# Kernel tuning notes

Hardware: AMD Instinct MI355X
Metric: run time of the kernel (lower is better)

## Reference

```python
import jax, jax.numpy as jnp
import numpy as np

DIM = 256
HEADS = 8
WSZ = (2, 7, 7)
SSZ = (1, 3, 3)
EPS = 1e-5


def _rel_index(wsz):
    wt, wh, ww = wsz
    coords = np.stack(np.meshgrid(np.arange(wt), np.arange(wh), np.arange(ww), indexing='ij'))
    coords = coords.reshape(3, -1)  # (3, N)
    rel = coords[:, :, None] - coords[:, None, :]  # (3, N, N)
    rel = rel.transpose(1, 2, 0).copy()  # (N, N, 3)
    rel[:, :, 0] += wt - 1
    rel[:, :, 1] += wh - 1
    rel[:, :, 2] += ww - 1
    rel[:, :, 0] *= (2 * wh - 1) * (2 * ww - 1)
    rel[:, :, 1] *= (2 * ww - 1)
    return rel.sum(-1)  # (N, N) int


def _attn_mask_np(T, H, W, wsz, ssz):
    wt, wh, ww = wsz
    st, sh, sw = ssz
    img = np.zeros((T, H, W), np.int32)
    cnt = 0
    for t in (slice(0, -wt), slice(-wt, -st), slice(-st, None)):
        for h in (slice(0, -wh), slice(-wh, -sh), slice(-sh, None)):
            for w in (slice(0, -ww), slice(-ww, -sw), slice(-sw, None)):
                img[t, h, w] = cnt
                cnt += 1
    m = img.reshape(T // wt, wt, H // wh, wh, W // ww, ww)
    m = m.transpose(0, 2, 4, 1, 3, 5).reshape(-1, wt * wh * ww)  # (nW, N)
    diff = m[:, :, None] - m[:, None, :]
    return np.where(diff != 0, -100.0, 0.0).astype(np.float32)  # (nW, N, N)


def _ln(x, w, b):
    mu = x.mean(-1, keepdims=True)
    var = jnp.mean((x - mu) ** 2, -1, keepdims=True)
    return (x - mu) * jax.lax.rsqrt(var + EPS) * w + b


def _window_partition(x, wsz):
    B, T, H, W, C = x.shape
    wt, wh, ww = wsz
    x = x.reshape(B, T // wt, wt, H // wh, wh, W // ww, ww, C)
    x = x.transpose(0, 1, 3, 5, 2, 4, 6, 7)
    return x.reshape(-1, wt * wh * ww, C)


def _window_reverse(xw, wsz, B, T, H, W):
    wt, wh, ww = wsz
    C = xw.shape[-1]
    x = xw.reshape(B, T // wt, H // wh, W // ww, wt, wh, ww, C)
    x = x.transpose(0, 1, 4, 2, 5, 3, 6, 7)
    return x.reshape(B, T, H, W, C)


def setup_inputs() -> dict:
    key = jax.random.key(0)
    ks = jax.random.split(key, 8)
    B, T, H, W = 2, 8, 56, 56
    d = DIM
    hid = 4 * d
    rpe_rows = (2 * WSZ[0] - 1) * (2 * WSZ[1] - 1) * (2 * WSZ[2] - 1)
    s = 0.02
    return {
        'x': jax.random.normal(ks[0], (B, T, H, W, d), jnp.float32),
        'norm1_w': jnp.ones((d,), jnp.float32),
        'norm1_b': jnp.zeros((d,), jnp.float32),
        'qkv_w': jax.random.normal(ks[1], (3 * d, d), jnp.float32) * s,
        'qkv_b': jnp.zeros((3 * d,), jnp.float32),
        'proj_w': jax.random.normal(ks[2], (d, d), jnp.float32) * s,
        'proj_b': jnp.zeros((d,), jnp.float32),
        'rpe_table': jax.random.normal(ks[3], (rpe_rows, HEADS), jnp.float32) * s,
        'norm2_w': jnp.ones((d,), jnp.float32),
        'norm2_b': jnp.zeros((d,), jnp.float32),
        'fc1_w': jax.random.normal(ks[4], (hid, d), jnp.float32) * s,
        'fc1_b': jnp.zeros((hid,), jnp.float32),
        'fc2_w': jax.random.normal(ks[5], (d, hid), jnp.float32) * s,
        'fc2_b': jnp.zeros((d,), jnp.float32),
    }


def reference(x, norm1_w, norm1_b, qkv_w, qkv_b, proj_w, proj_b, rpe_table,
              norm2_w, norm2_b, fc1_w, fc1_b, fc2_w, fc2_b):
    B, T, H, W, C = x.shape
    wt, wh, ww = WSZ
    N = wt * wh * ww
    hd = C // HEADS
    scale = hd ** -0.5

    shortcut = x
    h = _ln(x, norm1_w, norm1_b)
    # shifted branch: cyclic roll + mask
    h = jnp.roll(h, (-SSZ[0], -SSZ[1], -SSZ[2]), axis=(1, 2, 3))
    mask = jnp.asarray(_attn_mask_np(T, H, W, WSZ, SSZ))  # (nW, N, N)
    nW = mask.shape[0]

    xw = _window_partition(h, WSZ)  # (B*nW, N, C)
    Bw = xw.shape[0]

    qkv = xw @ qkv_w.T + qkv_b  # (Bw, N, 3C)
    qkv = qkv.reshape(Bw, N, 3, HEADS, hd).transpose(2, 0, 3, 1, 4)
    q, k, v = qkv[0], qkv[1], qkv[2]  # (Bw, H, N, hd)

    idx = _rel_index(WSZ)  # (N, N)
    bias = rpe_table[idx].transpose(2, 0, 1)  # (heads, N, N)

    attn = jnp.einsum('bhnd,bhmd->bhnm', q * scale, k) + bias[None]
    attn = attn.reshape(B, nW, HEADS, N, N) + mask[None, :, None]
    attn = jax.nn.softmax(attn, axis=-1).reshape(Bw, HEADS, N, N)

    out = jnp.einsum('bhnm,bhmd->bhnd', attn, v)
    out = out.transpose(0, 2, 1, 3).reshape(Bw, N, C)
    out = out @ proj_w.T + proj_b

    out = _window_reverse(out, WSZ, B, T, H, W)
    out = jnp.roll(out, (SSZ[0], SSZ[1], SSZ[2]), axis=(1, 2, 3))

    x = shortcut + out
    h2 = _ln(x, norm2_w, norm2_b)
    h2 = jax.nn.gelu(h2 @ fc1_w.T + fc1_b, approximate=False)
    h2 = h2 @ fc2_w.T + fc2_b
    return x + h2
```

## Files before the change

kernel.cpp:

```cpp
#include <hip/hip_runtime.h>
#include <math.h>

#define TOKENS 50176
#define NWIN   512
#define C_DIM  256

typedef __attribute__((ext_vector_type(8))) short short8;
typedef __attribute__((ext_vector_type(4))) float f32x4;

__device__ __forceinline__ unsigned short f2bf(float f) {
    unsigned int u = __builtin_bit_cast(unsigned int, f);
    u += 0x7fffu + ((u >> 16) & 1);
    return (unsigned short)(u >> 16);
}

__device__ __forceinline__ void gll16(const void* g, void* l) {
    __builtin_amdgcn_global_load_lds(
        (const __attribute__((address_space(1))) unsigned int*)g,
        (__attribute__((address_space(3))) unsigned int*)l, 16, 0, 0);
}

__device__ __forceinline__ int win_token_to_flat(int u) {
    int g = u / 98;
    int n = u - g * 98;
    int bb  = g >> 8;
    int rem = g & 255;
    int tb = rem >> 6, hb = (rem >> 3) & 7, wb = rem & 7;
    int dt = n / 49;
    int r2 = n - dt * 49;
    int dh = r2 / 7, dw = r2 - dh * 7;
    int t = tb * 2 + dt, h = hb * 7 + dh, w = wb * 7 + dw;
    int ts = (t + 1) & 7;
    int hs = h + 3; if (hs >= 56) hs -= 56;
    int wsx = w + 3; if (wsx >= 56) wsx -= 56;
    return ((bb * 8 + ts) * 56 + hs) * 56 + wsx;
}

__global__ __launch_bounds__(256) void cvt_kernel(
        const float* __restrict__ src, unsigned short* __restrict__ dst, int n) {
    int i = blockIdx.x * 256 + threadIdx.x;
    if (i < n) dst[i] = f2bf(src[i]);
}

__global__ __launch_bounds__(256) void bm_kernel(
        const float* __restrict__ rpe, float* __restrict__ bm) {
    int i = blockIdx.x * 256 + threadIdx.x;
    int c  = i % 112;
    int t1 = i / 112;
    int r  = t1 % 112;
    int t2 = t1 / 112;
    int head = t2 & 7;
    int cls  = t2 >> 3;
    float val;
    if (c >= 98) {
        val = -1e30f;
    } else if (r >= 98) {
        val = 0.f;
    } else {
        int dt = r / 49, rr = r - dt * 49, dh = rr / 7, dw = rr - dh * 7;
        int dt2 = c / 49, cc = c - dt2 * 49, dh2 = cc / 7, dw2 = cc - dh2 * 7;
        int rt  = (cls & 4) ? (dt  == 0 ? 1 : 2) : 0;
        int rh  = (cls & 2) ? (dh  <  4 ? 1 : 2) : 0;
        int rw  = (cls & 1) ? (dw  <  4 ? 1 : 2) : 0;
        int rt2 = (cls & 4) ? (dt2 == 0 ? 1 : 2) : 0;
        int rh2 = (cls & 2) ? (dh2 <  4 ? 1 : 2) : 0;
        int rw2 = (cls & 1) ? (dw2 <  4 ? 1 : 2) : 0;
        int reg1 = rt * 9 + rh * 3 + rw, reg2 = rt2 * 9 + rh2 * 3 + rw2;
        int idx = (dt - dt2 + 1) * 169 + (dh - dh2 + 6) * 13 + (dw - dw2 + 6);
        val = rpe[idx * 8 + head] + ((reg1 == reg2) ? 0.f : -100.f);
    }
    bm[i] = val;
}

template<bool GATHER>
__global__ __launch_bounds__(256) void ln_kernel(
        const float* __restrict__ x, const float* __restrict__ w,
        const float* __restrict__ b, unsigned short* __restrict__ out) {
    int token = blockIdx.x * 4 + (threadIdx.x >> 6);
    int lane  = threadIdx.x & 63;
    size_t so = GATHER ? (size_t)win_token_to_flat(token) * C_DIM
                       : (size_t)token * C_DIM;
    const float* src = x + so;
    float v[4];
    float sum = 0.f;
#pragma unroll
    for (int j = 0; j < 4; ++j) { v[j] = src[lane + 64 * j]; sum += v[j]; }
#pragma unroll
    for (int o = 32; o > 0; o >>= 1) sum += __shfl_xor(sum, o, 64);
    float mu = sum * (1.f / 256.f);
    float var = 0.f;
#pragma unroll
    for (int j = 0; j < 4; ++j) { float d = v[j] - mu; var += d * d; }
#pragma unroll
    for (int o = 32; o > 0; o >>= 1) var += __shfl_xor(var, o, 64);
    float rstd = rsqrtf(var * (1.f / 256.f) + 1e-5f);
    unsigned short* dst = out + (size_t)token * C_DIM;
#pragma unroll
    for (int j = 0; j < 4; ++j) {
        int c = lane + 64 * j;
        dst[c] = f2bf((v[j] - mu) * rstd * w[c] + b[c]);
    }
}

template<int EPI>
__global__ __launch_bounds__(256) void mfma_gemm(
        const unsigned short* __restrict__ A, const unsigned short* __restrict__ B,
        const float* __restrict__ bias, const float* __restrict__ res,
        void* __restrict__ Cout, int M, int N, int K) {
    __shared__ __attribute__((aligned(16))) unsigned short Asm[2][128 * 32];
    __shared__ __attribute__((aligned(16))) unsigned short Bsm[2][128 * 32];
    int tid = threadIdx.x;
    int wave = tid >> 6, lane = tid & 63;

    int nwg = gridDim.x * gridDim.y;
    int bid = blockIdx.y * gridDim.x + blockIdx.x;
    int swz = (bid & 7) * (nwg >> 3) + (bid >> 3);
    int bx = swz % gridDim.x, by = swz / gridDim.x;

    int row0 = by * 128, col0 = bx * 128;
    int wr = (wave >> 1) * 64;
    int wc = (wave & 1) * 64;

    f32x4 acc[4][4] = {};

    int sr = tid >> 2;
    int sk = (((tid & 3) ^ ((sr >> 2) & 3)) * 8);
    const unsigned short* Ag0 = A + (size_t)(row0 + sr) * K + sk;
    const unsigned short* Ag1 = A + (size_t)(row0 + 64 + sr) * K + sk;
    const unsigned short* Bg0 = B + (size_t)(col0 + sr) * K + sk;
    const unsigned short* Bg1 = B + (size_t)(col0 + 64 + sr) * K + sk;
    int loff = tid * 8;

    int fm = lane & 15, fq = lane >> 4;
    int fks = (fq ^ ((fm >> 2) & 3)) * 8;

    gll16(Ag0, &Asm[0][loff]);
    gll16(Ag1, &Asm[0][loff + 2048]);
    gll16(Bg0, &Bsm[0][loff]);
    gll16(Bg1, &Bsm[0][loff + 2048]);

    int nk = K >> 5;
    for (int s = 0; s < nk; ++s) {
        int cur = s & 1;
        __syncthreads();
        if (s + 1 < nk) {
            int k0 = (s + 1) << 5;
            gll16(Ag0 + k0, &Asm[cur ^ 1][loff]);
            gll16(Ag1 + k0, &Asm[cur ^ 1][loff + 2048]);
            gll16(Bg0 + k0, &Bsm[cur ^ 1][loff]);
            gll16(Bg1 + k0, &Bsm[cur ^ 1][loff + 2048]);
        }
        short8 af[4], bfr[4];
#pragma unroll
        for (int t4 = 0; t4 < 4; ++t4) {
            af[t4]  = *(const short8*)&Asm[cur][(wr + t4 * 16 + fm) * 32 + fks];
            bfr[t4] = *(const short8*)&Bsm[cur][(wc + t4 * 16 + fm) * 32 + fks];
        }
#pragma unroll
        for (int i = 0; i < 4; ++i)
#pragma unroll
            for (int j = 0; j < 4; ++j)
                acc[i][j] = __builtin_amdgcn_mfma_f32_16x16x32_bf16(
                    af[i], bfr[j], acc[i][j], 0, 0, 0);
    }

    int crow0 = row0 + wr + (lane >> 4) * 4;
    int ccol0 = col0 + wc + (lane & 15);
    float bj[4];
#pragma unroll
    for (int j = 0; j < 4; ++j) bj[j] = bias[ccol0 + j * 16];

    if (EPI == 0) {
        unsigned short* C = (unsigned short*)Cout;
        float mul = (col0 < 256) ? 0.17677669529663687f : 1.f;
#pragma unroll
        for (int i = 0; i < 4; ++i)
#pragma unroll
            for (int v = 0; v < 4; ++v) {
                size_t base = (size_t)(crow0 + i * 16 + v) * N + ccol0;
#pragma unroll
                for (int j = 0; j < 4; ++j)
                    C[base + j * 16] = f2bf((acc[i][j][v] + bj[j]) * mul);
            }
    } else if (EPI == 1) {
        float* C = (float*)Cout;
#pragma unroll
        for (int i = 0; i < 4; ++i)
#pragma unroll
            for (int v = 0; v < 4; ++v) {
                int r = crow0 + i * 16 + v;
                size_t base = (size_t)win_token_to_flat(r) * C_DIM + ccol0;
#pragma unroll
                for (int j = 0; j < 4; ++j)
                    C[base + j * 16] = res[base + j * 16] + acc[i][j][v] + bj[j];
            }
    } else if (EPI == 2) {
        unsigned short* C = (unsigned short*)Cout;
#pragma unroll
        for (int i = 0; i < 4; ++i)
#pragma unroll
            for (int v = 0; v < 4; ++v) {
                size_t base = (size_t)(crow0 + i * 16 + v) * N + ccol0;
#pragma unroll
                for (int j = 0; j < 4; ++j) {
                    float val = acc[i][j][v] + bj[j];
                    C[base + j * 16] =
                        f2bf(0.5f * val * (1.f + erff(val * 0.70710678118654752f)));
                }
            }
    } else {
        float* C = (float*)Cout;
#pragma unroll
        for (int i = 0; i < 4; ++i)
#pragma unroll
            for (int v = 0; v < 4; ++v) {
                size_t base = (size_t)(crow0 + i * 16 + v) * N + ccol0;
#pragma unroll
                for (int j = 0; j < 4; ++j)
                    C[base + j * 16] = res[base + j * 16] + acc[i][j][v] + bj[j];
            }
    }
}

__global__ __launch_bounds__(256) void attn_mfma_kernel(
        const unsigned short* __restrict__ qkv, const float* __restrict__ bm,
        unsigned short* __restrict__ out) {
    __shared__ __attribute__((aligned(16))) unsigned short Vt[32][136];
    __shared__ __attribute__((aligned(16))) unsigned short Pw[4][16][136];
    int blk = blockIdx.x;
    int g = blk >> 3, head = blk & 7;
    int tid = threadIdx.x, wave = tid >> 6, lane = tid & 63;

    for (int i = tid; i < 32 * 30; i += 256) {
        int d = i / 30, c = 98 + (i - d * 30);
        Vt[d][c] = 0;
    }
    const unsigned short* vbase = qkv + (size_t)g * 98 * 768 + 512 + head * 32;
    for (int i = tid; i < 98 * 16; i += 256) {
        int n = i >> 4, dp = i & 15;
        unsigned int val = *(const unsigned int*)(vbase + (size_t)n * 768 + dp * 2);
        Vt[dp * 2][n]     = (unsigned short)val;
        Vt[dp * 2 + 1][n] = (unsigned short)(val >> 16);
    }
    {
        int m = lane >> 2, c = 112 + (lane & 3) * 4;
        *(unsigned long long*)&Pw[wave][m][c] = 0ULL;
    }
    __syncthreads();

    const unsigned short* qbase = qkv + (size_t)g * 98 * 768 + head * 32;
    const unsigned short* kbase = qbase + 256;
    int rem = g & 255;
    int cls = (((rem >> 6) == 3) << 2) | (((((rem >> 3) & 7)) == 7) << 1) | ((rem & 7) == 7);
    const float* bmh = bm + (size_t)(cls * 8 + head) * 112 * 112;

    int fm = lane & 15, fq = lane >> 4;
    int fk = fq * 8;
    unsigned short* obase = out + (size_t)g * 98 * 256 + head * 32;

    for (int s = wave; s < 7; s += 4) {
        int m0 = s * 16;
        int arow = m0 + fm; if (arow > 97) arow = 97;
        short8 af = *(const short8*)(qbase + (size_t)arow * 768 + fk);
        f32x4 S[7];
        f32x4 z = {0.f, 0.f, 0.f, 0.f};
#pragma unroll
        for (int j = 0; j < 7; ++j) {
            int krow = j * 16 + fm; if (krow > 97) krow = 97;
            short8 kf = *(const short8*)(kbase + (size_t)krow * 768 + fk);
            S[j] = __builtin_amdgcn_mfma_f32_16x16x32_bf16(af, kf, z, 0, 0, 0);
        }
        const float* bmrow = bmh + (m0 + fq * 4) * 112 + fm;
#pragma unroll
        for (int j = 0; j < 7; ++j)
#pragma unroll
            for (int v = 0; v < 4; ++v)
                S[j][v] += bmrow[v * 112 + j * 16];
        float inv[4];
#pragma unroll
        for (int v = 0; v < 4; ++v) {
            float m_ = S[0][v];
#pragma unroll
            for (int j = 1; j < 7; ++j) m_ = fmaxf(m_, S[j][v]);
#pragma unroll
            for (int o = 1; o < 16; o <<= 1) m_ = fmaxf(m_, __shfl_xor(m_, o, 64));
            float t = 0.f;
#pragma unroll
            for (int j = 0; j < 7; ++j) { S[j][v] = __expf(S[j][v] - m_); t += S[j][v]; }
#pragma unroll
            for (int o = 1; o < 16; o <<= 1) t += __shfl_xor(t, o, 64);
            inv[v] = 1.f / t;
        }
#pragma unroll
        for (int j = 0; j < 7; ++j)
#pragma unroll
            for (int v = 0; v < 4; ++v)
                Pw[wave][fq * 4 + v][j * 16 + fm] = f2bf(S[j][v]);
        f32x4 O0 = {0.f, 0.f, 0.f, 0.f}, O1 = {0.f, 0.f, 0.f, 0.f};
#pragma unroll
        for (int ks = 0; ks < 4; ++ks) {
            short8 pf = *(const short8*)&Pw[wave][fm][ks * 32 + fk];
            short8 v0 = *(const short8*)&Vt[fm][ks * 32 + fk];
            short8 v1 = *(const short8*)&Vt[16 + fm][ks * 32 + fk];
            O0 = __builtin_amdgcn_mfma_f32_16x16x32_bf16(pf, v0, O0, 0, 0, 0);
            O1 = __builtin_amdgcn_mfma_f32_16x16x32_bf16(pf, v1, O1, 0, 0, 0);
        }
#pragma unroll
        for (int v = 0; v < 4; ++v) {
            int row = m0 + fq * 4 + v;
            if (row < 98) {
                obase[(size_t)row * 256 + fm]      = f2bf(O0[v] * inv[v]);
                obase[(size_t)row * 256 + 16 + fm] = f2bf(O1[v] * inv[v]);
            }
        }
    }
}

extern "C" void kernel_launch(void* const* d_in, const int* in_sizes, int n_in,
                              void* d_out, int out_size, void* d_ws, size_t ws_size,
                              hipStream_t stream) {
    const float* x     = (const float*)d_in[0];
    const float* n1w   = (const float*)d_in[1];
    const float* n1b   = (const float*)d_in[2];
    const float* qkvw  = (const float*)d_in[3];
    const float* qkvb  = (const float*)d_in[4];
    const float* projw = (const float*)d_in[5];
    const float* projb = (const float*)d_in[6];
    const float* rpe   = (const float*)d_in[7];
    const float* n2w   = (const float*)d_in[8];
    const float* n2b   = (const float*)d_in[9];
    const float* fc1w  = (const float*)d_in[10];
    const float* fc1b  = (const float*)d_in[11];
    const float* fc2w  = (const float*)d_in[12];
    const float* fc2b  = (const float*)d_in[13];
    float* out = (float*)d_out;

    unsigned short* wqkv  = (unsigned short*)d_ws;
    unsigned short* wproj = wqkv + 768 * 256;
    unsigned short* wfc1  = wproj + 256 * 256;
    unsigned short* wfc2  = wfc1 + 1024 * 256;
    float* bm = (float*)(wfc2 + 256 * 1024);
    unsigned short* actA  = (unsigned short*)(bm + 8 * 8 * 112 * 112);
    unsigned short* attnO = actA + (size_t)TOKENS * 256;
    unsigned short* qkv_bf = attnO + (size_t)TOKENS * 256;
    unsigned short* fc1o = qkv_bf;

    bm_kernel<<<8 * 8 * 112 * 112 / 256, 256, 0, stream>>>(rpe, bm);
    cvt_kernel<<<(768 * 256 + 255) / 256, 256, 0, stream>>>(qkvw, wqkv, 768 * 256);
    cvt_kernel<<<(256 * 256 + 255) / 256, 256, 0, stream>>>(projw, wproj, 256 * 256);
    cvt_kernel<<<(1024 * 256 + 255) / 256, 256, 0, stream>>>(fc1w, wfc1, 1024 * 256);
    cvt_kernel<<<(256 * 1024 + 255) / 256, 256, 0, stream>>>(fc2w, wfc2, 256 * 1024);

    ln_kernel<true><<<TOKENS / 4, 256, 0, stream>>>(x, n1w, n1b, actA);
    mfma_gemm<0><<<dim3(768 / 128, TOKENS / 128), 256, 0, stream>>>(
        actA, wqkv, qkvb, nullptr, qkv_bf, TOKENS, 768, 256);
    attn_mfma_kernel<<<NWIN * 8, 256, 0, stream>>>(qkv_bf, bm, attnO);
    mfma_gemm<1><<<dim3(256 / 128, TOKENS / 128), 256, 0, stream>>>(
        attnO, wproj, projb, x, out, TOKENS, 256, 256);
    ln_kernel<false><<<TOKENS / 4, 256, 0, stream>>>(out, n2w, n2b, actA);
    mfma_gemm<2><<<dim3(1024 / 128, TOKENS / 128), 256, 0, stream>>>(
        actA, wfc1, fc1b, nullptr, fc1o, TOKENS, 1024, 256);
    mfma_gemm<3><<<dim3(256 / 128, TOKENS / 128), 256, 0, stream>>>(
        fc1o, wfc2, fc2b, out, out, TOKENS, 256, 1024);
}
```

Measured before the change: 391.7 us.

## Deepen GEMM prefetch pipeline, drop LDS swizzle, use polynomial erf GELU

Restructures the GEMM main loop so two K-tiles are in flight at once. It waits with an explicit vmcnt, reads fragments into registers, then issues the next global-to-LDS load into the buffer just freed before running the MFMAs. The aim is to overlap global loads with compute and shorten the barrier stalls. It also removes the XOR swizzle on LDS rows, which may bring back bank conflicts on fragment reads. Separately, the GELU epilogue replaces erff with an Abramowitz-Stegun polynomial erf using a fast reciprocal and __expf, which is cheaper but slightly less accurate.

```diff
diff --git a/kernel.cpp b/kernel.cpp
--- a/kernel.cpp
+++ b/kernel.cpp
@@ -18,6 +18,17 @@
     __builtin_amdgcn_global_load_lds(
         (const __attribute__((address_space(1))) unsigned int*)g,
         (__attribute__((address_space(3))) unsigned int*)l, 16, 0, 0);
+}
+
+__device__ __forceinline__ float gelu_exact(float v) {
+    float z  = v * 0.70710678118654752f;
+    float az = fabsf(z);
+    float t  = __builtin_amdgcn_rcpf(1.f + 0.3275911f * az);
+    float p  = ((((1.061405429f * t - 1.453152027f) * t + 1.421413741f) * t
+                 - 0.284496736f) * t + 0.254829592f) * t;
+    float er = 1.f - p * __expf(-az * az);
+    er = (z < 0.f) ? -er : er;
+    return 0.5f * v * (1.f + er);
 }
 
 __device__ __forceinline__ int win_token_to_flat(int u) {
@@ -124,7 +135,7 @@
     f32x4 acc[4][4] = {};
 
     int sr = tid >> 2;
-    int sk = (((tid & 3) ^ ((sr >> 2) & 3)) * 8);
+    int sk = (tid & 3) * 8;
     const unsigned short* Ag0 = A + (size_t)(row0 + sr) * K + sk;
     const unsigned short* Ag1 = A + (size_t)(row0 + 64 + sr) * K + sk;
     const unsigned short* Bg0 = B + (size_t)(col0 + sr) * K + sk;
@@ -132,24 +143,51 @@
     int loff = tid * 8;
 
     int fm = lane & 15, fq = lane >> 4;
-    int fks = (fq ^ ((fm >> 2) & 3)) * 8;
-
-    gll16(Ag0, &Asm[0][loff]);
-    gll16(Ag1, &Asm[0][loff + 2048]);
-    gll16(Bg0, &Bsm[0][loff]);
-    gll16(Bg1, &Bsm[0][loff + 2048]);
+    int fks = fq * 8;
 
     int nk = K >> 5;
-    for (int s = 0; s < nk; ++s) {
+    {
+        gll16(Ag0, &Asm[0][loff]);
+        gll16(Ag1, &Asm[0][loff + 2048]);
+        gll16(Bg0, &Bsm[0][loff]);
+        gll16(Bg1, &Bsm[0][loff + 2048]);
+        gll16(Ag0 + 32, &Asm[1][loff]);
+        gll16(Ag1 + 32, &Asm[1][loff + 2048]);
+        gll16(Bg0 + 32, &Bsm[1][loff]);
+        gll16(Bg1 + 32, &Bsm[1][loff + 2048]);
+    }
+
+    for (int s = 0; s < nk - 1; ++s) {
         int cur = s & 1;
-        __syncthreads();
-        if (s + 1 < nk) {
-            int k0 = (s + 1) << 5;
-            gll16(Ag0 + k0, &Asm[cur ^ 1][loff]);
-            gll16(Ag1 + k0, &Asm[cur ^ 1][loff + 2048]);
-            gll16(Bg0 + k0, &Bsm[cur ^ 1][loff]);
-            gll16(Bg1 + k0, &Bsm[cur ^ 1][loff + 2048]);
-        }
+        asm volatile("s_waitcnt vmcnt(4)" ::: "memory");
+        __builtin_amdgcn_s_barrier();
+        short8 af[4], bfr[4];
+#pragma unroll
+        for (int t4 = 0; t4 < 4; ++t4) {
+            af[t4]  = *(const short8*)&Asm[cur][(wr + t4 * 16 + fm) * 32 + fks];
+            bfr[t4] = *(const short8*)&Bsm[cur][(wc + t4 * 16 + fm) * 32 + fks];
+        }
+        asm volatile("s_waitcnt lgkmcnt(0)" ::: "memory");
+        __builtin_amdgcn_sched_barrier(0);
+        __builtin_amdgcn_s_barrier();
+        if (s + 2 < nk) {
+            int k0 = (s + 2) << 5;
+            gll16(Ag0 + k0, &Asm[cur][loff]);
+            gll16(Ag1 + k0, &Asm[cur][loff + 2048]);
+            gll16(Bg0 + k0, &Bsm[cur][loff]);
+            gll16(Bg1 + k0, &Bsm[cur][loff + 2048]);
+        }
+#pragma unroll
+        for (int i = 0; i < 4; ++i)
+#pragma unroll
+            for (int j = 0; j < 4; ++j)
+                acc[i][j] = __builtin_amdgcn_mfma_f32_16x16x32_bf16(
+                    af[i], bfr[j], acc[i][j], 0, 0, 0);
+    }
+    {
+        int cur = (nk - 1) & 1;
+        asm volatile("s_waitcnt vmcnt(0)" ::: "memory");
+        __builtin_amdgcn_s_barrier();
         short8 af[4], bfr[4];
 #pragma unroll
         for (int t4 = 0; t4 < 4; ++t4) {
@@ -202,11 +240,8 @@
             for (int v = 0; v < 4; ++v) {
                 size_t base = (size_t)(crow0 + i * 16 + v) * N + ccol0;
 #pragma unroll
-                for (int j = 0; j < 4; ++j) {
-                    float val = acc[i][j][v] + bj[j];
-                    C[base + j * 16] =
-                        f2bf(0.5f * val * (1.f + erff(val * 0.70710678118654752f)));
-                }
+                for (int j = 0; j < 4; ++j)
+                    C[base + j * 16] = f2bf(gelu_exact(acc[i][j][v] + bj[j]));
             }
     } else {
         float* C = (float*)Cout;
```

Result: slower. 409.1 us (+4.4%).

## Use register-direct MFMA GEMM for K=256 layers, polynomial GELU, drop LDS swizzle

Applied to the files above, without the earlier changes.

Adds a GEMM kernel for the K=256 GEMMs (qkv, proj, fc1) that loads A and B fragments straight from global memory into registers, fully unrolled over K, with no LDS staging and no block barriers. Each wave computes a 32x128 tile, and launch bounds request two blocks per CU. The fc1 epilogue replaces erff with a rational-polynomial erf approximation (Abramowitz-Stegun style) to cut transcendental cost. It also removes the XOR swizzle in the remaining LDS GEMM (fc2), which may add bank conflicts there, and B-tile reuse now relies on the caches rather than shared memory.

```diff
diff --git a/kernel.cpp b/kernel.cpp
--- a/kernel.cpp
+++ b/kernel.cpp
@@ -18,6 +18,17 @@
     __builtin_amdgcn_global_load_lds(
         (const __attribute__((address_space(1))) unsigned int*)g,
         (__attribute__((address_space(3))) unsigned int*)l, 16, 0, 0);
+}
+
+__device__ __forceinline__ float gelu_exact(float v) {
+    float z  = v * 0.70710678118654752f;
+    float az = fabsf(z);
+    float t  = __builtin_amdgcn_rcpf(1.f + 0.3275911f * az);
+    float p  = ((((1.061405429f * t - 1.453152027f) * t + 1.421413741f) * t
+                 - 0.284496736f) * t + 0.254829592f) * t;
+    float er = 1.f - p * __expf(-az * az);
+    er = (z < 0.f) ? -er : er;
+    return 0.5f * v * (1.f + er);
 }
 
 __device__ __forceinline__ int win_token_to_flat(int u) {
@@ -102,6 +113,87 @@
     }
 }
 
+template<int EPI, int K>
+__global__ __launch_bounds__(256, 2) void rt_gemm(
+        const unsigned short* __restrict__ A, const unsigned short* __restrict__ B,
+        const float* __restrict__ bias, const float* __restrict__ res,
+        void* __restrict__ Cout, int M, int N) {
+    int tid = threadIdx.x;
+    int wave = tid >> 6, lane = tid & 63;
+
+    int nwg = gridDim.x * gridDim.y;
+    int bid = blockIdx.y * gridDim.x + blockIdx.x;
+    int swz = (bid & 7) * (nwg >> 3) + (bid >> 3);
+    int bx = swz % gridDim.x, by = swz / gridDim.x;
+
+    int row0 = by * 128 + wave * 32;
+    int col0 = bx * 128;
+
+    int fm = lane & 15, fq = lane >> 4;
+    const unsigned short* Ap = A + (size_t)(row0 + fm) * K + fq * 8;
+    const unsigned short* Bp = B + (size_t)(col0 + fm) * K + fq * 8;
+
+    f32x4 acc[2][8] = {};
+
+#pragma unroll
+    for (int kk = 0; kk < K; kk += 32) {
+        short8 a0 = *(const short8*)(Ap + kk);
+        short8 a1 = *(const short8*)(Ap + (size_t)16 * K + kk);
+        short8 bfr[8];
+#pragma unroll
+        for (int j = 0; j < 8; ++j)
+            bfr[j] = *(const short8*)(Bp + (size_t)j * 16 * K + kk);
+#pragma unroll
+        for (int j = 0; j < 8; ++j) {
+            acc[0][j] = __builtin_amdgcn_mfma_f32_16x16x32_bf16(a0, bfr[j], acc[0][j], 0, 0, 0);
+            acc[1][j] = __builtin_amdgcn_mfma_f32_16x16x32_bf16(a1, bfr[j], acc[1][j], 0, 0, 0);
+        }
+    }
+
+    float bj[8];
+#pragma unroll
+    for (int j = 0; j < 8; ++j) bj[j] = bias[col0 + j * 16 + fm];
+
+    if (EPI == 0) {
+        unsigned short* C = (unsigned short*)Cout;
+        float mul = (col0 < 256) ? 0.17677669529663687f : 1.f;
+#pragma unroll
+        for (int i = 0; i < 2; ++i)
+#pragma unroll
+            for (int v = 0; v < 4; ++v) {
+                int r = row0 + i * 16 + fq * 4 + v;
+                size_t base = (size_t)r * N + col0 + fm;
+#pragma unroll
+                for (int j = 0; j < 8; ++j)
+                    C[base + j * 16] = f2bf((acc[i][j][v] + bj[j]) * mul);
+            }
+    } else if (EPI == 1) {
+        float* C = (float*)Cout;
+#pragma unroll
+        for (int i = 0; i < 2; ++i)
+#pragma unroll
+            for (int v = 0; v < 4; ++v) {
+                int r = row0 + i * 16 + fq * 4 + v;
+                size_t base = (size_t)win_token_to_flat(r) * C_DIM + col0 + fm;
+#pragma unroll
+                for (int j = 0; j < 8; ++j)
+                    C[base + j * 16] = res[base + j * 16] + acc[i][j][v] + bj[j];
+            }
+    } else {
+        unsigned short* C = (unsigned short*)Cout;
+#pragma unroll
+        for (int i = 0; i < 2; ++i)
+#pragma unroll
+            for (int v = 0; v < 4; ++v) {
+                int r = row0 + i * 16 + fq * 4 + v;
+                size_t base = (size_t)r * N + col0 + fm;
+#pragma unroll
+                for (int j = 0; j < 8; ++j)
+                    C[base + j * 16] = f2bf(gelu_exact(acc[i][j][v] + bj[j]));
+            }
+    }
+}
+
 template<int EPI>
 __global__ __launch_bounds__(256) void mfma_gemm(
         const unsigned short* __restrict__ A, const unsigned short* __restrict__ B,
@@ -124,7 +216,7 @@
     f32x4 acc[4][4] = {};
 
     int sr = tid >> 2;
-    int sk = (((tid & 3) ^ ((sr >> 2) & 3)) * 8);
+    int sk = (tid & 3) * 8;
     const unsigned short* Ag0 = A + (size_t)(row0 + sr) * K + sk;
     const unsigned short* Ag1 = A + (size_t)(row0 + 64 + sr) * K + sk;
     const unsigned short* Bg0 = B + (size_t)(col0 + sr) * K + sk;
@@ -132,7 +224,7 @@
     int loff = tid * 8;
 
     int fm = lane & 15, fq = lane >> 4;
-    int fks = (fq ^ ((fm >> 2) & 3)) * 8;
+    int fks = fq * 8;
 
     gll16(Ag0, &Asm[0][loff]);
     gll16(Ag1, &Asm[0][loff + 2048]);
@@ -170,45 +262,7 @@
 #pragma unroll
     for (int j = 0; j < 4; ++j) bj[j] = bias[ccol0 + j * 16];
 
-    if (EPI == 0) {
-        unsigned short* C = (unsigned short*)Cout;
-        float mul = (col0 < 256) ? 0.17677669529663687f : 1.f;
-#pragma unroll
-        for (int i = 0; i < 4; ++i)
-#pragma unroll
-            for (int v = 0; v < 4; ++v) {
-                size_t base = (size_t)(crow0 + i * 16 + v) * N + ccol0;
-#pragma unroll
-                for (int j = 0; j < 4; ++j)
-                    C[base + j * 16] = f2bf((acc[i][j][v] + bj[j]) * mul);
-            }
-    } else if (EPI == 1) {
-        float* C = (float*)Cout;
-#pragma unroll
-        for (int i = 0; i < 4; ++i)
-#pragma unroll
-            for (int v = 0; v < 4; ++v) {
-                int r = crow0 + i * 16 + v;
-                size_t base = (size_t)win_token_to_flat(r) * C_DIM + ccol0;
-#pragma unroll
-                for (int j = 0; j < 4; ++j)
-                    C[base + j * 16] = res[base + j * 16] + acc[i][j][v] + bj[j];
-            }
-    } else if (EPI == 2) {
-        unsigned short* C = (unsigned short*)Cout;
-#pragma unroll
-        for (int i = 0; i < 4; ++i)
-#pragma unroll
-            for (int v = 0; v < 4; ++v) {
-                size_t base = (size_t)(crow0 + i * 16 + v) * N + ccol0;
-#pragma unroll
-                for (int j = 0; j < 4; ++j) {
-                    float val = acc[i][j][v] + bj[j];
-                    C[base + j * 16] =
-                        f2bf(0.5f * val * (1.f + erff(val * 0.70710678118654752f)));
-                }
-            }
-    } else {
+    {
         float* C = (float*)Cout;
 #pragma unroll
         for (int i = 0; i < 4; ++i)
@@ -352,14 +406,14 @@
     cvt_kernel<<<(256 * 1024 + 255) / 256, 256, 0, stream>>>(fc2w, wfc2, 256 * 1024);
 
     ln_kernel<true><<<TOKENS / 4, 256, 0, stream>>>(x, n1w, n1b, actA);
-    mfma_gemm<0><<<dim3(768 / 128, TOKENS / 128), 256, 0, stream>>>(
-        actA, wqkv, qkvb, nullptr, qkv_bf, TOKENS, 768, 256);
+    rt_gemm<0, 256><<<dim3(768 / 128, TOKENS / 128), 256, 0, stream>>>(
+        actA, wqkv, qkvb, nullptr, qkv_bf, TOKENS, 768);
     attn_mfma_kernel<<<NWIN * 8, 256, 0, stream>>>(qkv_bf, bm, attnO);
-    mfma_gemm<1><<<dim3(256 / 128, TOKENS / 128), 256, 0, stream>>>(
-        attnO, wproj, projb, x, out, TOKENS, 256, 256);
+    rt_gemm<1, 256><<<dim3(256 / 128, TOKENS / 128), 256, 0, stream>>>(
+        attnO, wproj, projb, x, out, TOKENS, 256);
     ln_kernel<false><<<TOKENS / 4, 256, 0, stream>>>(out, n2w, n2b, actA);
-    mfma_gemm<2><<<dim3(1024 / 128, TOKENS / 128), 256, 0, stream>>>(
-        actA, wfc1, fc1b, nullptr, fc1o, TOKENS, 1024, 256);
+    rt_gemm<2, 256><<<dim3(1024 / 128, TOKENS / 128), 256, 0, stream>>>(
+        actA, wfc1, fc1b, nullptr, fc1o, TOKENS, 1024);
     mfma_gemm<3><<<dim3(256 / 128, TOKENS / 128), 256, 0, stream>>>(
         fc1o, wfc2, fc2b, out, out, TOKENS, 256, 1024);
 }
```

New measurement: 541.3 us. +38.2%, slower.

## Stage GEMM epilogues through LDS for coalesced stores, fast GELU, merge weight conversions

Applied to the files above, without the earlier changes.

GEMM epilogues now write results into shared memory and then store to global with wide coalesced vector writes, including vectorised residual adds for fp32 outputs. Exact erf-based GELU is replaced with a polynomial erf approximation, and the four weight-conversion launches are merged into one kernel. The LDS XOR swizzle on the operand tiles is removed, which may add bank conflicts in the main loop; extra barriers are added in the epilogue.

```diff
diff --git a/kernel.cpp b/kernel.cpp
--- a/kernel.cpp
+++ b/kernel.cpp
@@ -18,6 +18,17 @@
     __builtin_amdgcn_global_load_lds(
         (const __attribute__((address_space(1))) unsigned int*)g,
         (__attribute__((address_space(3))) unsigned int*)l, 16, 0, 0);
+}
+
+__device__ __forceinline__ float gelu_exact(float v) {
+    float z  = v * 0.70710678118654752f;
+    float az = fabsf(z);
+    float t  = __builtin_amdgcn_rcpf(1.f + 0.3275911f * az);
+    float p  = ((((1.061405429f * t - 1.453152027f) * t + 1.421413741f) * t
+                 - 0.284496736f) * t + 0.254829592f) * t;
+    float er = 1.f - p * __expf(-az * az);
+    er = (z < 0.f) ? -er : er;
+    return 0.5f * v * (1.f + er);
 }
 
 __device__ __forceinline__ int win_token_to_flat(int u) {
@@ -36,10 +47,16 @@
     return ((bb * 8 + ts) * 56 + hs) * 56 + wsx;
 }
 
-__global__ __launch_bounds__(256) void cvt_kernel(
-        const float* __restrict__ src, unsigned short* __restrict__ dst, int n) {
+__global__ __launch_bounds__(256) void cvt_all_kernel(
+        const float* __restrict__ s0, const float* __restrict__ s1,
+        const float* __restrict__ s2, const float* __restrict__ s3,
+        unsigned short* __restrict__ d0, unsigned short* __restrict__ d1,
+        unsigned short* __restrict__ d2, unsigned short* __restrict__ d3) {
     int i = blockIdx.x * 256 + threadIdx.x;
-    if (i < n) dst[i] = f2bf(src[i]);
+    if (i < 196608)      d0[i] = f2bf(s0[i]);
+    else if (i < 262144) d1[i - 196608] = f2bf(s1[i - 196608]);
+    else if (i < 524288) d2[i - 262144] = f2bf(s2[i - 262144]);
+    else                 d3[i - 524288] = f2bf(s3[i - 524288]);
 }
 
 __global__ __launch_bounds__(256) void bm_kernel(
@@ -107,8 +124,9 @@
         const unsigned short* __restrict__ A, const unsigned short* __restrict__ B,
         const float* __restrict__ bias, const float* __restrict__ res,
         void* __restrict__ Cout, int M, int N, int K) {
-    __shared__ __attribute__((aligned(16))) unsigned short Asm[2][128 * 32];
-    __shared__ __attribute__((aligned(16))) unsigned short Bsm[2][128 * 32];
+    __shared__ __attribute__((aligned(16))) unsigned short smem[4][128 * 32];
+#define ASMB(b) (smem[(b)])
+#define BSMB(b) (smem[2 + (b)])
     int tid = threadIdx.x;
     int wave = tid >> 6, lane = tid & 63;
 
@@ -124,7 +142,7 @@
     f32x4 acc[4][4] = {};
 
     int sr = tid >> 2;
-    int sk = (((tid & 3) ^ ((sr >> 2) & 3)) * 8);
+    int sk = (tid & 3) * 8;
     const unsigned short* Ag0 = A + (size_t)(row0 + sr) * K + sk;
     const unsigned short* Ag1 = A + (size_t)(row0 + 64 + sr) * K + sk;
     const unsigned short* Bg0 = B + (size_t)(col0 + sr) * K + sk;
@@ -132,12 +150,12 @@
     int loff = tid * 8;
 
     int fm = lane & 15, fq = lane >> 4;
-    int fks = (fq ^ ((fm >> 2) & 3)) * 8;
-
-    gll16(Ag0, &Asm[0][loff]);
-    gll16(Ag1, &Asm[0][loff + 2048]);
-    gll16(Bg0, &Bsm[0][loff]);
-    gll16(Bg1, &Bsm[0][loff + 2048]);
+    int fks = fq * 8;
+
+    gll16(Ag0, &ASMB(0)[loff]);
+    gll16(Ag1, &ASMB(0)[loff + 2048]);
+    gll16(Bg0, &BSMB(0)[loff]);
+    gll16(Bg1, &BSMB(0)[loff + 2048]);
 
     int nk = K >> 5;
     for (int s = 0; s < nk; ++s) {
@@ -145,16 +163,16 @@
         __syncthreads();
         if (s + 1 < nk) {
             int k0 = (s + 1) << 5;
-            gll16(Ag0 + k0, &Asm[cur ^ 1][loff]);
-            gll16(Ag1 + k0, &Asm[cur ^ 1][loff + 2048]);
-            gll16(Bg0 + k0, &Bsm[cur ^ 1][loff]);
-            gll16(Bg1 + k0, &Bsm[cur ^ 1][loff + 2048]);
+            gll16(Ag0 + k0, &ASMB(cur ^ 1)[loff]);
+            gll16(Ag1 + k0, &ASMB(cur ^ 1)[loff + 2048]);
+            gll16(Bg0 + k0, &BSMB(cur ^ 1)[loff]);
+            gll16(Bg1 + k0, &BSMB(cur ^ 1)[loff + 2048]);
         }
         short8 af[4], bfr[4];
 #pragma unroll
         for (int t4 = 0; t4 < 4; ++t4) {
-            af[t4]  = *(const short8*)&Asm[cur][(wr + t4 * 16 + fm) * 32 + fks];
-            bfr[t4] = *(const short8*)&Bsm[cur][(wc + t4 * 16 + fm) * 32 + fks];
+            af[t4]  = *(const short8*)&ASMB(cur)[(wr + t4 * 16 + fm) * 32 + fks];
+            bfr[t4] = *(const short8*)&BSMB(cur)[(wc + t4 * 16 + fm) * 32 + fks];
         }
 #pragma unroll
         for (int i = 0; i < 4; ++i)
@@ -164,62 +182,74 @@
                     af[i], bfr[j], acc[i][j], 0, 0, 0);
     }
 
-    int crow0 = row0 + wr + (lane >> 4) * 4;
-    int ccol0 = col0 + wc + (lane & 15);
+    int ccol0 = col0 + wc + fm;
     float bj[4];
 #pragma unroll
     for (int j = 0; j < 4; ++j) bj[j] = bias[ccol0 + j * 16];
 
-    if (EPI == 0) {
-        unsigned short* C = (unsigned short*)Cout;
-        float mul = (col0 < 256) ? 0.17677669529663687f : 1.f;
+    __syncthreads();
+
+    if (EPI == 0 || EPI == 2) {
+        unsigned short* Ls = &smem[0][0];
+        float mul = (EPI == 0 && col0 < 256) ? 0.17677669529663687f : 1.f;
 #pragma unroll
         for (int i = 0; i < 4; ++i)
 #pragma unroll
             for (int v = 0; v < 4; ++v) {
-                size_t base = (size_t)(crow0 + i * 16 + v) * N + ccol0;
-#pragma unroll
-                for (int j = 0; j < 4; ++j)
-                    C[base + j * 16] = f2bf((acc[i][j][v] + bj[j]) * mul);
-            }
-    } else if (EPI == 1) {
-        float* C = (float*)Cout;
-#pragma unroll
-        for (int i = 0; i < 4; ++i)
-#pragma unroll
-            for (int v = 0; v < 4; ++v) {
-                int r = crow0 + i * 16 + v;
-                size_t base = (size_t)win_token_to_flat(r) * C_DIM + ccol0;
-#pragma unroll
-                for (int j = 0; j < 4; ++j)
-                    C[base + j * 16] = res[base + j * 16] + acc[i][j][v] + bj[j];
-            }
-    } else if (EPI == 2) {
-        unsigned short* C = (unsigned short*)Cout;
-#pragma unroll
-        for (int i = 0; i < 4; ++i)
-#pragma unroll
-            for (int v = 0; v < 4; ++v) {
-                size_t base = (size_t)(crow0 + i * 16 + v) * N + ccol0;
+                int lr = wr + i * 16 + fq * 4 + v;
 #pragma unroll
                 for (int j = 0; j < 4; ++j) {
                     float val = acc[i][j][v] + bj[j];
-                    C[base + j * 16] =
-                        f2bf(0.5f * val * (1.f + erff(val * 0.70710678118654752f)));
+                    val = (EPI == 2) ? gelu_exact(val) : val * mul;
+                    Ls[lr * 128 + wc + j * 16 + fm] = f2bf(val);
                 }
             }
+        __syncthreads();
+        unsigned short* C = (unsigned short*)Cout;
+#pragma unroll
+        for (int p = 0; p < 8; ++p) {
+            int lin = p * 2048 + tid * 8;
+            int lr = lin >> 7, lc = lin & 127;
+            *(short8*)(C + (size_t)(row0 + lr) * N + col0 + lc) =
+                *(const short8*)&Ls[lin];
+        }
     } else {
+        float* fs = (float*)&smem[0][0];
         float* C = (float*)Cout;
 #pragma unroll
-        for (int i = 0; i < 4; ++i)
-#pragma unroll
-            for (int v = 0; v < 4; ++v) {
-                size_t base = (size_t)(crow0 + i * 16 + v) * N + ccol0;
-#pragma unroll
-                for (int j = 0; j < 4; ++j)
-                    C[base + j * 16] = res[base + j * 16] + acc[i][j][v] + bj[j];
+        for (int h = 0; h < 2; ++h) {
+            if (h) __syncthreads();
+            if (wr == h * 64) {
+#pragma unroll
+                for (int i = 0; i < 4; ++i)
+#pragma unroll
+                    for (int v = 0; v < 4; ++v) {
+                        int lr = i * 16 + fq * 4 + v;
+#pragma unroll
+                        for (int j = 0; j < 4; ++j)
+                            fs[lr * 128 + wc + j * 16 + fm] = acc[i][j][v] + bj[j];
+                    }
             }
-    }
+            __syncthreads();
+            int tr = tid >> 2, tcb = (tid & 3) * 32;
+            int grow = row0 + h * 64 + tr;
+            size_t gbase = (EPI == 1)
+                ? (size_t)win_token_to_flat(grow) * C_DIM + col0 + tcb
+                : (size_t)grow * N + col0 + tcb;
+            const float* rs = res + gbase;
+            float* Cp = C + gbase;
+            const float* ls = &fs[tr * 128 + tcb];
+#pragma unroll
+            for (int q = 0; q < 8; ++q) {
+                f32x4 r = *(const f32x4*)(rs + q * 4);
+                f32x4 a = *(const f32x4*)(ls + q * 4);
+                r.x += a.x; r.y += a.y; r.z += a.z; r.w += a.w;
+                *(f32x4*)(Cp + q * 4) = r;
+            }
+        }
+    }
+#undef ASMB
+#undef BSMB
 }
 
 __global__ __launch_bounds__(256) void attn_mfma_kernel(
@@ -346,10 +376,8 @@
     unsigned short* fc1o = qkv_bf;
 
     bm_kernel<<<8 * 8 * 112 * 112 / 256, 256, 0, stream>>>(rpe, bm);
-    cvt_kernel<<<(768 * 256 + 255) / 256, 256, 0, stream>>>(qkvw, wqkv, 768 * 256);
-    cvt_kernel<<<(256 * 256 + 255) / 256, 256, 0, stream>>>(projw, wproj, 256 * 256);
-    cvt_kernel<<<(1024 * 256 + 255) / 256, 256, 0, stream>>>(fc1w, wfc1, 1024 * 256);
-    cvt_kernel<<<(256 * 1024 + 255) / 256, 256, 0, stream>>>(fc2w, wfc2, 256 * 1024);
+    cvt_all_kernel<<<786432 / 256, 256, 0, stream>>>(
+        qkvw, projw, fc1w, fc2w, wqkv, wproj, wfc1, wfc2);
 
     ln_kernel<true><<<TOKENS / 4, 256, 0, stream>>>(x, n1w, n1b, actA);
     mfma_gemm<0><<<dim3(768 / 128, TOKENS / 128), 256, 0, stream>>>(
```

After: 382.5 us. -2.4%, faster.
